# Optimization experiments

Hardware: AMD Instinct MI355X
Metric: run time of the kernel (lower is better)

The kernel has to match this reference:

```python
import jax, jax.numpy as jnp
import numpy as np

B, C, IC, H, W = 16, 256, 128, 32, 32  # batch, in_channels, inter_channels, spatial
EPS = 1e-5


def _conv1x1(x, w, b=None):
    # x: [B,C,H,W], w: [O,C] -> [B,O,H,W]
    y = jnp.einsum('bchw,oc->bohw', x, w)
    if b is not None:
        y = y + b[None, :, None, None]
    return y


def _dot_kernel(x, wt, wp):
    # relu-matmul attention, symmetrized, degree-rsqrt normalized with zero masking
    b, _, h, w = x.shape
    n = h * w
    t = jnp.maximum(_conv1x1(x, wt), 0.0).reshape(b, -1, n)  # [B,IC,N]
    p = jnp.maximum(_conv1x1(x, wp), 0.0).reshape(b, -1, n)  # [B,IC,N]
    att = jnp.einsum('bcn,bcm->bnm', t, p)                    # [B,N,N]
    att = (att + att.transpose(0, 2, 1)) * 0.5
    d = att.sum(axis=2)                                       # [B,N]
    dinv = jnp.where(d != 0, jax.lax.rsqrt(jnp.where(d != 0, d, 1.0)), 0.0)
    return att * dinv[:, None, :] * dinv[:, :, None]


def _bn(x, gamma, beta):
    # BatchNorm2d in training mode (batch statistics, biased variance)
    mu = jnp.mean(x, axis=(0, 2, 3), keepdims=True)
    var = jnp.mean((x - mu) ** 2, axis=(0, 2, 3), keepdims=True)
    xhat = (x - mu) * jax.lax.rsqrt(var + EPS)
    return xhat * gamma[None, :, None, None] + beta[None, :, None, None]


def setup_inputs() -> dict:
    key = jax.random.key(0)
    ks = jax.random.split(key, 32)
    s = 0.05
    inp = {
        'x':  jax.random.normal(ks[0], (B, C, H, W), jnp.float32),
        'ob': jax.random.normal(ks[1], (B, C, H, W), jnp.float32),
        'od': jax.random.normal(ks[2], (B, C, H, W), jnp.float32),
        'Wt': jax.random.normal(ks[3], (IC, C), jnp.float32) * s,
        'Wp': jax.random.normal(ks[4], (IC, C), jnp.float32) * s,
        'Wgx': jax.random.normal(ks[5], (IC, C), jnp.float32) * s,
        'bgx': jax.random.normal(ks[6], (IC,), jnp.float32) * s,
        'Wgb': jax.random.normal(ks[7], (IC, C), jnp.float32) * s,
        'bgb': jax.random.normal(ks[8], (IC,), jnp.float32) * s,
        'Wgd': jax.random.normal(ks[9], (IC, C), jnp.float32) * s,
        'bgd': jax.random.normal(ks[10], (IC,), jnp.float32) * s,
        'Wwx': jax.random.normal(ks[11], (C, IC), jnp.float32) * s,
        'bwx': jax.random.normal(ks[12], (C,), jnp.float32) * s,
        'Wwb': jax.random.normal(ks[13], (C, IC), jnp.float32) * s,
        'bwb': jax.random.normal(ks[14], (C,), jnp.float32) * s,
        'Wwd': jax.random.normal(ks[15], (C, IC), jnp.float32) * s,
        'bwd': jax.random.normal(ks[16], (C,), jnp.float32) * s,
        'Wwxb': jax.random.normal(ks[17], (C, IC), jnp.float32) * s,
        'bwxb': jax.random.normal(ks[18], (C,), jnp.float32) * s,
        'Wwxd': jax.random.normal(ks[19], (C, IC), jnp.float32) * s,
        'bwxd': jax.random.normal(ks[20], (C,), jnp.float32) * s,
        'gamma1': jnp.ones((C,), jnp.float32),
        'beta1': jnp.zeros((C,), jnp.float32),
        'gamma2': jnp.ones((C,), jnp.float32),
        'beta2': jnp.zeros((C,), jnp.float32),
        'Wout': jax.random.normal(ks[21], (C, C), jnp.float32) * s,
        'bout': jax.random.normal(ks[22], (C,), jnp.float32) * s,
    }
    return inp


def reference(x, ob, od, Wt, Wp, Wgx, bgx, Wgb, bgb, Wgd, bgd,
              Wwx, bwx, Wwb, bwb, Wwd, bwd, Wwxb, bwxb, Wwxd, bwxd,
              gamma1, beta1, gamma2, beta2, Wout, bout):
    b, c, h, w = x.shape
    n = h * w

    def g_tokens(inp, wg, bg):
        return _conv1x1(inp, wg, bg).reshape(b, -1, n).transpose(0, 2, 1)  # [B,N,IC]

    g_x = g_tokens(x, Wgx, bgx)
    g_b = g_tokens(ob, Wgb, bgb)
    g_d = g_tokens(od, Wgd, bgd)

    f_x = _dot_kernel(x, Wt, Wp)
    f_b = _dot_kernel(ob, Wt, Wp)
    f_d = _dot_kernel(od, Wt, Wp)

    def agg(f, g):
        # bmm(f,g).transpose(1,2).view(B,IC,H,W)
        return jnp.einsum('bnm,bmi->bin', f, g).reshape(b, -1, h, w)

    x_self = _conv1x1(agg(f_x, g_x), Wwx, bwx)
    ob_self = _conv1x1(agg(f_b, g_b), Wwb, bwb)
    od_self = _conv1x1(agg(f_d, g_d), Wwd, bwd)
    x_ob_cross = _conv1x1(agg(f_b, g_x), Wwxb, bwxb)
    x_od_cross = _conv1x1(agg(f_d, g_x), Wwxd, bwxd)

    od_final = _bn(od_self + x_ob_cross, gamma1, beta1)
    ob_final = _bn(ob_self + x_od_cross, gamma2, beta2)
    output = _conv1x1(od_final + ob_final + x_self, Wout, bout)
    return output + x
```

## Files before the change

kernel.cpp:

```cpp
#include <hip/hip_runtime.h>

#define GAS __attribute__((address_space(1)))
#define LAS __attribute__((address_space(3)))

typedef __attribute__((ext_vector_type(8))) short short8;
typedef __attribute__((ext_vector_type(4))) short short4_t;
typedef __attribute__((ext_vector_type(4))) float f32x4;
typedef unsigned short u16;

constexpr int cB = 16, cC = 256, cIC = 128, cN = 1024;

__device__ __forceinline__ u16 f2bf(float v) {
    unsigned u = __builtin_bit_cast(unsigned, v);
    return (u16)((u + 0x7fffu + ((u >> 16) & 1u)) >> 16);
}
__device__ __forceinline__ float bf2f(u16 v) {
    unsigned u = ((unsigned)v) << 16;
    return __builtin_bit_cast(float, u);
}
__device__ __forceinline__ float rsz(float d) {
    return (d != 0.0f) ? rsqrtf(d) : 0.0f;
}

template<int N> __device__ __forceinline__ void wait_vmcnt() {
    if constexpr (N == 0) asm volatile("s_waitcnt vmcnt(0)" ::: "memory");
    else if constexpr (N == 1) asm volatile("s_waitcnt vmcnt(1)" ::: "memory");
    else if constexpr (N == 2) asm volatile("s_waitcnt vmcnt(2)" ::: "memory");
    else if constexpr (N == 3) asm volatile("s_waitcnt vmcnt(3)" ::: "memory");
    else if constexpr (N == 4) asm volatile("s_waitcnt vmcnt(4)" ::: "memory");
    else if constexpr (N == 5) asm volatile("s_waitcnt vmcnt(5)" ::: "memory");
    else if constexpr (N == 6) asm volatile("s_waitcnt vmcnt(6)" ::: "memory");
    else if constexpr (N == 8) asm volatile("s_waitcnt vmcnt(8)" ::: "memory");
}

template<int BM, int BN, int WR, int WC, bool BREMAP = false>
__device__ __forceinline__ void gemm_core(
    const u16* __restrict__ Ab, const u16* __restrict__ Ab2, int ksplit, int lda,
    const u16* __restrict__ Bb, int ldb, int K,
    u16* lsA, u16* lsB,
    f32x4 (&acc)[BM/(WR*16)][BN/(WC*16)])
{
    constexpr int THREADS = WR * WC * 64;
    constexpr int MR = BM / (WR * 16), NR = BN / (WC * 16);
    constexpr int ACH = (BM * 64) / (THREADS * 16);
    constexpr int BCH = (BN * 64) / (THREADS * 16);
    constexpr int RPC = THREADS / 4;
    constexpr int ISSUES = ACH + BCH;

    const int tid  = threadIdx.x;
    const int lane = tid & 63;
    const int wave = tid >> 6;
    const int wr = wave / WC, wc = wave % WC;
    const int r0 = tid >> 2, slot = tid & 3;

    auto stage = [&](int buf, int kk) {
        const u16* Ak = (Ab2 != nullptr && kk >= ksplit) ? (Ab2 + (kk - ksplit)) : (Ab + kk);
        const u16* Bk = Bb + (BREMAP ? (((kk >> 7) << 8) + (kk & 127)) : kk);
        #pragma unroll
        for (int c = 0; c < ACH; c++) {
            int row = c * RPC + r0;
            int sk = (slot ^ ((row >> 1) & 3)) << 3;
            __builtin_amdgcn_global_load_lds((GAS void*)(Ak + (size_t)row * lda + sk),
                (LAS void*)(lsA + buf * (BM * 32) + c * (THREADS * 8) + (wave << 9)), 16, 0, 0);
        }
        #pragma unroll
        for (int c = 0; c < BCH; c++) {
            int row = c * RPC + r0;
            int sk = (slot ^ ((row >> 1) & 3)) << 3;
            __builtin_amdgcn_global_load_lds((GAS void*)(Bk + (size_t)row * ldb + sk),
                (LAS void*)(lsB + buf * (BN * 32) + c * (THREADS * 8) + (wave << 9)), 16, 0, 0);
        }
    };

    stage(0, 0);
    const int nt = K >> 5;
    for (int t = 0; t < nt; t++) {
        const int cur = t & 1;
        if (t + 1 < nt) { stage(cur ^ 1, (t + 1) << 5); wait_vmcnt<ISSUES>(); }
        else            wait_vmcnt<0>();
        __builtin_amdgcn_s_barrier();
        asm volatile("" ::: "memory");

        const u16* la = lsA + cur * (BM * 32);
        const u16* lb = lsB + cur * (BN * 32);
        short8 af[MR], bf[NR];
        #pragma unroll
        for (int m = 0; m < MR; m++) {
            int row = wr * (BM / WR) + (m << 4) + (lane & 15);
            af[m] = *(const short8*)&la[(row << 5) + (((lane >> 4) ^ ((row >> 1) & 3)) << 3)];
        }
        #pragma unroll
        for (int n = 0; n < NR; n++) {
            int row = wc * (BN / WC) + (n << 4) + (lane & 15);
            bf[n] = *(const short8*)&lb[(row << 5) + (((lane >> 4) ^ ((row >> 1) & 3)) << 3)];
        }
        #pragma unroll
        for (int m = 0; m < MR; m++)
            #pragma unroll
            for (int n = 0; n < NR; n++)
                acc[m][n] = __builtin_amdgcn_mfma_f32_16x16x32_bf16(af[m], bf[n], acc[m][n], 0, 0, 0);

        asm volatile("s_waitcnt lgkmcnt(0)" ::: "memory");
        __builtin_amdgcn_sched_barrier(0);
        __builtin_amdgcn_s_barrier();
    }
}

template<int BM, int BN, int WR, int WC, bool RELU, bool OBF16, bool RBIAS, bool RESID>
__global__ __launch_bounds__(WR*WC*64) void gemm_bt(
    const u16* __restrict__ A, long long sA, long long sA2, int lda,
    const u16* __restrict__ B, long long sB, long long sB2, int ldb,
    void* __restrict__ C, long long sC, long long sC2, int ldc,
    int K,
    const float* __restrict__ bias, int sb2,
    const float* __restrict__ resid, long long sR)
{
    __shared__ alignas(16) u16 lsA[2 * BM * 32];
    __shared__ alignas(16) u16 lsB[2 * BN * 32];

    const int lane = threadIdx.x & 63;
    const int wave = threadIdx.x >> 6;
    const int wr = wave / WC, wc = wave % WC;
    const int zlo = blockIdx.z & 15, zhi = blockIdx.z >> 4;

    const u16* Ab = A + zlo * sA + zhi * sA2 + (size_t)(blockIdx.x * BM) * lda;
    const u16* Bb = B + zlo * sB + zhi * sB2 + (size_t)(blockIdx.y * BN) * ldb;

    f32x4 acc[BM/(WR*16)][BN/(WC*16)] = {};
    gemm_core<BM, BN, WR, WC>(Ab, nullptr, K, lda, Bb, ldb, K, lsA, lsB, acc);

    const int rowb = blockIdx.x * BM + wr * (BM / WR) + ((lane >> 4) << 2);
    const int colb = blockIdx.y * BN + wc * (BN / WC) + (lane & 15);
    const long long cbase = zlo * sC + zhi * sC2;
    #pragma unroll
    for (int m = 0; m < BM/(WR*16); m++) {
        #pragma unroll
        for (int n = 0; n < BN/(WC*16); n++) {
            #pragma unroll
            for (int r = 0; r < 4; r++) {
                int row = rowb + m * 16 + r;
                int col = colb + n * 16;
                float v = acc[m][n][r];
                if (RBIAS) v += bias[zhi * sb2 + row];
                if (RESID) v += resid[zlo * sR + (size_t)row * ldc + col];
                if (RELU)  v = fmaxf(v, 0.0f);
                if (OBF16) ((u16*)C)[cbase + (size_t)row * ldc + col] = f2bf(v);
                else       ((float*)C)[cbase + (size_t)row * ldc + col] = v;
            }
        }
    }
}

__global__ __launch_bounds__(512) void tp_gemm(
    const u16* __restrict__ XT, const u16* __restrict__ WTP,
    u16* __restrict__ TP, float* __restrict__ CS)
{
    __shared__ alignas(16) u16 lsA[2 * 128 * 32];
    __shared__ alignas(16) u16 lsB[2 * 256 * 32];

    const int nx = blockIdx.x, z = blockIdx.z;
    const u16* Ab = XT + (size_t)z * 262144 + (size_t)(nx * 128) * 256;

    f32x4 acc[4][4] = {};
    gemm_core<128, 256, 2, 4>(Ab, nullptr, 256, 256, WTP, 256, 256, lsA, lsB, acc);

    const int lane = threadIdx.x & 63;
    const int wave = threadIdx.x >> 6;
    const int wr = wave >> 2, wc = wave & 3;
    const int rowb = nx * 128 + wr * 64 + ((lane >> 4) << 2);
    const int colb = wc * 64 + (lane & 15);
    u16* Cb = TP + (size_t)z * 262144;

    float cp[4] = {};
    #pragma unroll
    for (int m = 0; m < 4; m++)
        #pragma unroll
        for (int n = 0; n < 4; n++)
            #pragma unroll
            for (int r = 0; r < 4; r++) {
                float v = fmaxf(acc[m][n][r], 0.0f);
                Cb[(size_t)(rowb + m * 16 + r) * 256 + colb + n * 16] = f2bf(v);
                cp[n] += v;
            }
    #pragma unroll
    for (int n = 0; n < 4; n++) {
        float v = cp[n];
        v += __shfl_xor(v, 16, 64);
        v += __shfl_xor(v, 32, 64);
        if (lane < 16)
            atomicAdd(&CS[z * 256 + colb + n * 16], v);
    }
}

__global__ __launch_bounds__(256) void tp_transpose(
    const u16* __restrict__ TP, const float* __restrict__ CS,
    u16* __restrict__ TPt, float* __restrict__ DINV)
{
    __shared__ u16 ls[64][68];
    __shared__ float ws[64];
    __shared__ float pd[4][64];

    const int z = blockIdx.z;
    const int n0 = blockIdx.x << 6, c0 = blockIdx.y << 6;
    const int tid = threadIdx.x;

    if (tid < 64) ws[tid] = 0.5f * CS[z * 256 + ((c0 + tid) ^ 128)];

    const u16* src = TP + (size_t)z * 262144;
    #pragma unroll
    for (int p = 0; p < 2; p++) {
        int nl = p * 32 + (tid >> 3);
        int c8 = (tid & 7) << 3;
        short8 v = *(const short8*)&src[(size_t)(n0 + nl) * 256 + c0 + c8];
        #pragma unroll
        for (int j = 0; j < 8; j++) ls[c8 + j][nl] = (u16)v[j];
    }
    __syncthreads();

    u16* dst = TPt + (size_t)z * 262144;
    #pragma unroll
    for (int p = 0; p < 2; p++) {
        int cl = p * 32 + (tid >> 3);
        int n8 = (tid & 7) << 3;
        short4_t o0, o1;
        #pragma unroll
        for (int j = 0; j < 4; j++) { o0[j] = (short)ls[cl][n8 + j]; o1[j] = (short)ls[cl][n8 + 4 + j]; }
        *(short4_t*)&dst[(size_t)(c0 + cl) * 1024 + n0 + n8] = o0;
        *(short4_t*)&dst[(size_t)(c0 + cl) * 1024 + n0 + n8 + 4] = o1;
    }

    const int n = tid & 63, q = tid >> 6;
    float a = 0;
    #pragma unroll
    for (int c = 0; c < 16; c++) a += bf2f(ls[q * 16 + c][n]) * ws[q * 16 + c];
    pd[q][n] = a;
    __syncthreads();
    if (tid < 64)
        atomicAdd(&DINV[(z << 10) + n0 + tid],
                  pd[0][tid] + pd[1][tid] + pd[2][tid] + pd[3][tid]);
}

__global__ __launch_bounds__(256) void g_gemm(
    const u16* __restrict__ XT, const u16* __restrict__ WG,
    const float* __restrict__ BG, const float* __restrict__ DINV,
    u16* __restrict__ GXp, u16* __restrict__ GBp, u16* __restrict__ GDp)
{
    __shared__ alignas(16) u16 lsA[2 * 128 * 32];
    __shared__ alignas(16) u16 lsB[2 * 128 * 32];

    const int yb = blockIdx.x, zs = blockIdx.z;
    const int stream = zs >> 4, b = zs & 15;

    const u16* Ab = WG + stream * 32768;
    const u16* Bb = XT + (size_t)zs * 262144 + (size_t)(yb * 128) * 256;

    f32x4 acc[4][4] = {};
    gemm_core<128, 128, 2, 2>(Ab, nullptr, 256, 256, Bb, 256, 256, lsA, lsB, acc);

    const int lane = threadIdx.x & 63;
    const int wave = threadIdx.x >> 6;
    const int wr = wave >> 1, wc = wave & 1;
    const int rowb = (wr << 6) + ((lane >> 4) << 2);
    const int colb = yb * 128 + (wc << 6) + (lane & 15);
    const float* dvx = DINV + (b << 10);
    const float* dvb = DINV + 16384 + (b << 10);
    const float* dvd = DINV + 32768 + (b << 10);
    float sx[4], sb_[4], sd[4];
    #pragma unroll
    for (int n = 0; n < 4; n++) {
        int col = colb + n * 16;
        if (stream == 0) { sx[n] = rsz(dvx[col]); sb_[n] = rsz(dvb[col]); sd[n] = rsz(dvd[col]); }
        else if (stream == 1) sb_[n] = rsz(dvb[col]);
        else sd[n] = rsz(dvd[col]);
    }
    #pragma unroll
    for (int m = 0; m < 4; m++) {
        #pragma unroll
        for (int r = 0; r < 4; r++) {
            int row = rowb + m * 16 + r;
            float bias = BG[stream * 128 + row];
            #pragma unroll
            for (int n = 0; n < 4; n++) {
                int col = colb + n * 16;
                float v = acc[m][n][r] + bias;
                if (stream == 0) {
                    GXp[(size_t)b * 131072 + ((size_t)row << 10) + col] = f2bf(v * sx[n]);
                    GBp[(size_t)b * 262144 + ((size_t)(row + 128) << 10) + col] = f2bf(v * sb_[n]);
                    GDp[(size_t)b * 262144 + ((size_t)(row + 128) << 10) + col] = f2bf(v * sd[n]);
                } else if (stream == 1) {
                    GBp[(size_t)b * 262144 + ((size_t)row << 10) + col] = f2bf(v * sb_[n]);
                } else {
                    GDp[(size_t)b * 262144 + ((size_t)row << 10) + col] = f2bf(v * sd[n]);
                }
            }
        }
    }
}

__global__ __launch_bounds__(256) void inner_splitk(
    const u16* __restrict__ TPt, const u16* __restrict__ GXp,
    const u16* __restrict__ GBp, const u16* __restrict__ GDp,
    u16* __restrict__ MX, u16* __restrict__ MB, u16* __restrict__ MD)
{
    __shared__ alignas(16) u16 lsA[2 * 128 * 32];
    __shared__ alignas(16) u16 lsB[2 * 128 * 32];

    const int bz = blockIdx.z;
    const int split = bz / 48, z = bz % 48;
    const int which = z >> 4, b = z & 15;
    if (which == 0 && blockIdx.y) return;
    const u16* Gp = (which == 0) ? GXp : (which == 1) ? GBp : GDp;
    u16* M = (which == 0) ? MX : (which == 1) ? MB : MD;
    const int JD  = (which == 0) ? 128 : 256;
    const int ldc = 2 * JD;
    const long long sB = (which == 0) ? 131072 : 262144;

    const u16* Ab = TPt + (size_t)z * 262144 + (size_t)(blockIdx.x * 128) * 1024 + split * 512;
    const u16* Bb = Gp + (size_t)b * sB + (size_t)(blockIdx.y * 128) * 1024 + split * 512;

    f32x4 acc[4][4] = {};
    gemm_core<128, 128, 2, 2>(Ab, nullptr, 512, 1024, Bb, 1024, 512, lsA, lsB, acc);

    const int lane = threadIdx.x & 63;
    const int wave = threadIdx.x >> 6;
    const int wr = wave >> 1, wc = wave & 1;
    const int rowb = blockIdx.x * 128 + (wr << 6) + ((lane >> 4) << 2);
    const int colb = blockIdx.y * 128 + (wc << 6) + (lane & 15);
    u16* Cb = M + (size_t)b * (256 * ldc);
    #pragma unroll
    for (int m = 0; m < 4; m++)
        #pragma unroll
        for (int n = 0; n < 4; n++)
            #pragma unroll
            for (int r = 0; r < 4; r++) {
                int row = (rowb + m * 16 + r) ^ 128;
                int col = split * JD + colb + n * 16;
                Cb[(size_t)row * ldc + col] = f2bf(acc[m][n][r]);
            }
}

__global__ __launch_bounds__(512) void fold_gemm(
    const u16* __restrict__ WF2, const u16* __restrict__ MX,
    const u16* __restrict__ MB, const u16* __restrict__ MD,
    u16* __restrict__ FF2)
{
    __shared__ alignas(16) u16 lsA[2 * 128 * 32];
    __shared__ alignas(16) u16 lsB[2 * 256 * 32];

    const int z = blockIdx.z, q = z >> 4, b = z & 15;
    const int pr = (q == 4) ? 2 : (q >> 1);
    const int side = (q == 1 || q == 3) ? 1 : 0;

    const u16* Ab = WF2 + q * 65536 + (size_t)(blockIdx.x * 128) * 256;

    f32x4 acc[4][4] = {};
    if (q == 4) {
        const u16* Bb = MX + (size_t)b * 65536;
        gemm_core<128, 256, 2, 4, false>(Ab, nullptr, 256, 256, Bb, 256, 256, lsA, lsB, acc);
    } else {
        const u16* Mp = (q == 1 || q == 2) ? MB : MD;
        const int coff = side ? 128 : 0;
        const u16* Bb = Mp + (size_t)b * 131072 + coff;
        gemm_core<128, 256, 2, 4, true>(Ab, nullptr, 256, 256, Bb, 512, 256, lsA, lsB, acc);
    }

    const int lane = threadIdx.x & 63;
    const int wave = threadIdx.x >> 6;
    const int wr = wave >> 2, wc = wave & 3;
    const int rowb = blockIdx.x * 128 + wr * 64 + ((lane >> 4) << 2);
    const int colb = wc * 64 + (lane & 15);
    u16* Cb = FF2 + (size_t)pr * 2097152 + (size_t)b * 131072;
    #pragma unroll
    for (int m = 0; m < 4; m++)
        #pragma unroll
        for (int n = 0; n < 4; n++)
            #pragma unroll
            for (int r = 0; r < 4; r++)
                Cb[(size_t)(rowb + m * 16 + r) * 512 + side * 256 + colb + n * 16]
                    = f2bf(acc[m][n][r]);
}

__global__ __launch_bounds__(512) void outer_gemm(
    const u16* __restrict__ TP, const u16* __restrict__ FF2,
    const float* __restrict__ DINV,
    u16* __restrict__ SALL, float* __restrict__ BNA)
{
    __shared__ alignas(16) u16 lsA[2 * 128 * 32];
    __shared__ alignas(16) u16 lsB[2 * 256 * 32];

    const int z = blockIdx.z, zhi = z >> 4, b = z & 15;
    const int sa1[3] = {2, 1, 0}, sa2[3] = {1, 2, 0};

    const int lane = threadIdx.x & 63;
    const int wave = threadIdx.x >> 6;
    const int wr = wave >> 2, wc = wave & 3;
    const int rowb = blockIdx.x * 128 + wr * 64 + ((lane >> 4) << 2);
    const int colb = wc * 64 + (lane & 15);

    const u16* A1 = TP + (size_t)(sa1[zhi] * 16 + b) * 262144 + (size_t)(blockIdx.x * 128) * 256;
    const u16* B1 = FF2 + (size_t)zhi * 2097152 + (size_t)b * 131072;
    const float* dv1 = DINV + sa1[zhi] * 16384 + (b << 10);

    f32x4 acc[4][4] = {};
    gemm_core<128, 256, 2, 4>(A1, nullptr, 256, 256, B1, 512, 256, lsA, lsB, acc);

    f32x4 keep[4][4];
    #pragma unroll
    for (int m = 0; m < 4; m++) {
        f32x4 dva;
        #pragma unroll
        for (int r = 0; r < 4; r++) dva[r] = rsz(dv1[rowb + m * 16 + r]);
        #pragma unroll
        for (int n = 0; n < 4; n++) keep[m][n] = acc[m][n] * dva;
    }

    if (zhi < 2) {
        const u16* A2 = TP + (size_t)(sa2[zhi] * 16 + b) * 262144 + (size_t)(blockIdx.x * 128) * 256;
        const u16* B2 = B1 + 256;
        const float* dv2 = DINV + sa2[zhi] * 16384 + (b << 10);
        #pragma unroll
        for (int m = 0; m < 4; m++)
            #pragma unroll
            for (int n = 0; n < 4; n++) acc[m][n] = f32x4{0.f, 0.f, 0.f, 0.f};
        gemm_core<128, 256, 2, 4>(A2, nullptr, 256, 256, B2, 512, 256, lsA, lsB, acc);
        #pragma unroll
        for (int m = 0; m < 4; m++) {
            f32x4 dva;
            #pragma unroll
            for (int r = 0; r < 4; r++) dva[r] = rsz(dv2[rowb + m * 16 + r]);
            #pragma unroll
            for (int n = 0; n < 4; n++) keep[m][n] = keep[m][n] + acc[m][n] * dva;
        }
    }

    u16* Cb = SALL + (size_t)b * 786432;
    float csum[4] = {}, csq[4] = {};
    #pragma unroll
    for (int m = 0; m < 4; m++)
        #pragma unroll
        for (int n = 0; n < 4; n++)
            #pragma unroll
            for (int r = 0; r < 4; r++) {
                float v = keep[m][n][r];
                Cb[(size_t)(rowb + m * 16 + r) * 768 + zhi * 256 + colb + n * 16] = f2bf(v);
                csum[n] += v;
                csq[n] += v * v;
            }
    if (zhi < 2) {
        #pragma unroll
        for (int n = 0; n < 4; n++) {
            float s = csum[n], q = csq[n];
            s += __shfl_xor(s, 16, 64); s += __shfl_xor(s, 32, 64);
            q += __shfl_xor(q, 16, 64); q += __shfl_xor(q, 32, 64);
            if (lane < 16) {
                atomicAdd(&BNA[zhi * 512 + colb + n * 16], s);
                atomicAdd(&BNA[zhi * 512 + 256 + colb + n * 16], q);
            }
        }
    }
}

__global__ __launch_bounds__(256) void bnscale(
    const float* __restrict__ Wout, const float* __restrict__ g1, const float* __restrict__ be1,
    const float* __restrict__ g2, const float* __restrict__ be2,
    const float* __restrict__ bwx, const float* __restrict__ bout,
    const float* __restrict__ BNA, u16* __restrict__ WoutS, float* __restrict__ BIAS2)
{
    int o = blockIdx.x, c = threadIdx.x;
    const float inv = 1.0f / 16384.0f;
    float m1 = BNA[c] * inv;
    float v1 = BNA[256 + c] * inv - m1 * m1;
    float sc1 = g1[c] * rsqrtf(v1 + 1e-5f), sh1 = be1[c] - m1 * sc1;
    float m2 = BNA[512 + c] * inv;
    float v2 = BNA[768 + c] * inv - m2 * m2;
    float sc2 = g2[c] * rsqrtf(v2 + 1e-5f), sh2 = be2[c] - m2 * sc2;
    float wv = Wout[o * 256 + c];
    WoutS[o * 768 + c]       = f2bf(wv * sc1);
    WoutS[o * 768 + 256 + c] = f2bf(wv * sc2);
    WoutS[o * 768 + 512 + c] = f2bf(wv);
    __shared__ float red[256];
    red[c] = wv * (sh1 + sh2 + bwx[c]);
    __syncthreads();
    for (int s = 128; s; s >>= 1) { if (c < s) red[c] += red[c + s]; __syncthreads(); }
    if (c == 0) BIAS2[o] = red[0] + bout[o];
}

__global__ __launch_bounds__(256) void prep_transpose(
    const float* __restrict__ x, const float* __restrict__ ob,
    const float* __restrict__ od, u16* __restrict__ xt,
    const float* Wt, const float* Wp,
    const float* Wgx, const float* Wgb, const float* Wgd,
    const float* bgx, const float* bgb, const float* bgd,
    const float* Wwd, const float* Wwxb, const float* Wwb,
    const float* Wwxd, const float* Wwx,
    u16* wtp, u16* wg, u16* wf2, float* bg,
    float* __restrict__ ZZ)
{
    const int tid = threadIdx.x;
    if (blockIdx.z == 48) {
        int base = (blockIdx.y * 16 + blockIdx.x) * 1024;
        #pragma unroll
        for (int l = 0; l < 4; l++) {
            int t = base + l * 256 + tid;
            wtp[t] = f2bf(t < 32768 ? Wt[t] : Wp[t - 32768]);
            if (t < 32768) {
                wg[t] = f2bf(Wgx[t]); wg[32768 + t] = f2bf(Wgb[t]); wg[65536 + t] = f2bf(Wgd[t]);
            }
            {
                int o = t >> 8, k = t & 255, j = k & 127;
                const float* Wq[5] = {Wwd, Wwxb, Wwb, Wwxd, Wwx};
                #pragma unroll
                for (int q = 0; q < 5; q++)
                    wf2[q * 65536 + t] = f2bf(0.5f * Wq[q][o * 128 + j]);
            }
            if (t < 384) bg[t] = (t < 128) ? bgx[t] : (t < 256) ? bgb[t - 128] : bgd[t - 256];
            if (t < 62464) ZZ[t] = 0.0f;
        }
        return;
    }
    __shared__ float ls[64][68];
    const int z = blockIdx.z, which = z >> 4, b = z & 15;
    const float* src = (which == 0) ? x : (which == 1) ? ob : od;
    const float* s = src + (size_t)b * cC * cN;
    u16* dst = xt + (size_t)z * (cN * cC);
    const int n0 = blockIdx.x << 6, c0 = blockIdx.y << 6;

    const int cl0 = tid >> 4, n4 = (tid & 15) << 2;
    #pragma unroll
    for (int p = 0; p < 4; p++) {
        int cl = cl0 + (p << 4);
        f32x4 v = *(const f32x4*)&s[(size_t)(c0 + cl) * cN + n0 + n4];
        ls[cl][n4] = v[0]; ls[cl][n4 + 1] = v[1]; ls[cl][n4 + 2] = v[2]; ls[cl][n4 + 3] = v[3];
    }
    __syncthreads();
    const int nl0 = tid >> 3, c8 = (tid & 7) << 3;
    #pragma unroll
    for (int q = 0; q < 2; q++) {
        int nl = nl0 + (q << 5);
        short8 o;
        #pragma unroll
        for (int j = 0; j < 8; j++) o[j] = (short)f2bf(ls[c8 + j][nl]);
        *(short8*)&dst[(size_t)(n0 + nl) * 256 + c0 + c8] = o;
    }
}

extern "C" void kernel_launch(void* const* d_in, const int* in_sizes, int n_in,
                              void* d_out, int out_size, void* d_ws, size_t ws_size,
                              hipStream_t stream)
{
    const float* x    = (const float*)d_in[0];
    const float* ob   = (const float*)d_in[1];
    const float* od   = (const float*)d_in[2];
    const float* Wt   = (const float*)d_in[3];
    const float* Wp   = (const float*)d_in[4];
    const float* Wgx  = (const float*)d_in[5];
    const float* bgx  = (const float*)d_in[6];
    const float* Wgb  = (const float*)d_in[7];
    const float* bgb  = (const float*)d_in[8];
    const float* Wgd  = (const float*)d_in[9];
    const float* bgd  = (const float*)d_in[10];
    const float* Wwx  = (const float*)d_in[11];
    const float* bwx  = (const float*)d_in[12];
    const float* Wwb  = (const float*)d_in[13];
    const float* Wwd  = (const float*)d_in[15];
    const float* Wwxb = (const float*)d_in[17];
    const float* Wwxd = (const float*)d_in[19];
    const float* g1   = (const float*)d_in[21];
    const float* be1  = (const float*)d_in[22];
    const float* g2   = (const float*)d_in[23];
    const float* be2  = (const float*)d_in[24];
    const float* Wout = (const float*)d_in[25];
    const float* bout = (const float*)d_in[26];
    float* out = (float*)d_out;

    char* w = (char*)d_ws;
    u16*   XT    = (u16*)(w);
    u16*   TPt   = (u16*)(w + 25165824);
    u16*   TP    = (u16*)(w + 50331648);
    u16*   GXp   = (u16*)(w + 75497472);
    u16*   GBp   = (u16*)(w + 79691776);
    u16*   GDp   = (u16*)(w + 88080384);
    u16*   MX    = (u16*)(w + 96468992);
    u16*   MB    = (u16*)(w + 98566144);
    u16*   MD    = (u16*)(w + 102760448);
    u16*   FF2   = (u16*)(w + 106954752);
    u16*   WTP   = (u16*)(w + 119537664);
    u16*   WG    = (u16*)(w + 119668736);
    u16*   WF2   = (u16*)(w + 119865344);
    u16*   WoutS = (u16*)(w + 120520704);
    float* BGf   = (float*)(w + 120913920);
    float* BIAS2 = (float*)(w + 120915968);
    float* ZZ    = (float*)(w + 120920064);

    float* CS   = ZZ;
    float* BNA  = ZZ + 12288;
    float* DINV = ZZ + 13312;
    u16*   SALL = TPt;

    prep_transpose<<<dim3(16, 4, 49), 256, 0, stream>>>(
        x, ob, od, XT, Wt, Wp, Wgx, Wgb, Wgd, bgx, bgb, bgd,
        Wwd, Wwxb, Wwb, Wwxd, Wwx, WTP, WG, WF2, BGf, ZZ);

    tp_gemm<<<dim3(8, 1, 48), 512, 0, stream>>>(XT, WTP, TP, CS);

    tp_transpose<<<dim3(16, 4, 48), 256, 0, stream>>>(TP, CS, TPt, DINV);

    g_gemm<<<dim3(8, 1, 48), 256, 0, stream>>>(XT, WG, BGf, DINV, GXp, GBp, GDp);

    inner_splitk<<<dim3(2, 2, 96), 256, 0, stream>>>(TPt, GXp, GBp, GDp, MX, MB, MD);

    fold_gemm<<<dim3(2, 1, 80), 512, 0, stream>>>(WF2, MX, MB, MD, FF2);

    outer_gemm<<<dim3(8, 1, 48), 512, 0, stream>>>(TP, FF2, DINV, SALL, BNA);

    bnscale<<<dim3(256), 256, 0, stream>>>(Wout, g1, be1, g2, be2, bwx, bout,
                                           BNA, WoutS, BIAS2);

    gemm_bt<128, 128, 2, 2, false, false, true, true><<<dim3(2, 8, 16), 256, 0, stream>>>(
        WoutS, 0, 0, 768,  SALL, 786432, 0, 768,  out, 262144, 0, 1024,
        768, BIAS2, 0, x, 262144);
}
```

Before: 145.3 us.

## Fold degree normalization into transposed T/P buffers and split-K final GEMM with atomics

The per-row degree scale is now applied once, in a new per-row-tile transpose kernel that computes the full channel dot product locally. That kernel writes pre-scaled T/P in both layouts, which removes the DINV atomics, the scaling epilogues in g_gemm and outer_gemm, and lets outer_gemm run one fused two-source GEMM. The final output GEMM is split along K into two halves that atomically add into an output buffer pre-seeded with x during the prep pass, which doubles the block count. The trade-offs are extra bf16 rounding of the scaled operands, an extra full copy of x to the output, and atomic-add traffic on the output.

```diff
diff --git a/kernel.cpp b/kernel.cpp
--- a/kernel.cpp
+++ b/kernel.cpp
@@ -4,7 +4,6 @@
 #define LAS __attribute__((address_space(3)))
 
 typedef __attribute__((ext_vector_type(8))) short short8;
-typedef __attribute__((ext_vector_type(4))) short short4_t;
 typedef __attribute__((ext_vector_type(4))) float f32x4;
 typedef unsigned short u16;
 
@@ -106,51 +105,6 @@
     }
 }
 
-template<int BM, int BN, int WR, int WC, bool RELU, bool OBF16, bool RBIAS, bool RESID>
-__global__ __launch_bounds__(WR*WC*64) void gemm_bt(
-    const u16* __restrict__ A, long long sA, long long sA2, int lda,
-    const u16* __restrict__ B, long long sB, long long sB2, int ldb,
-    void* __restrict__ C, long long sC, long long sC2, int ldc,
-    int K,
-    const float* __restrict__ bias, int sb2,
-    const float* __restrict__ resid, long long sR)
-{
-    __shared__ alignas(16) u16 lsA[2 * BM * 32];
-    __shared__ alignas(16) u16 lsB[2 * BN * 32];
-
-    const int lane = threadIdx.x & 63;
-    const int wave = threadIdx.x >> 6;
-    const int wr = wave / WC, wc = wave % WC;
-    const int zlo = blockIdx.z & 15, zhi = blockIdx.z >> 4;
-
-    const u16* Ab = A + zlo * sA + zhi * sA2 + (size_t)(blockIdx.x * BM) * lda;
-    const u16* Bb = B + zlo * sB + zhi * sB2 + (size_t)(blockIdx.y * BN) * ldb;
-
-    f32x4 acc[BM/(WR*16)][BN/(WC*16)] = {};
-    gemm_core<BM, BN, WR, WC>(Ab, nullptr, K, lda, Bb, ldb, K, lsA, lsB, acc);
-
-    const int rowb = blockIdx.x * BM + wr * (BM / WR) + ((lane >> 4) << 2);
-    const int colb = blockIdx.y * BN + wc * (BN / WC) + (lane & 15);
-    const long long cbase = zlo * sC + zhi * sC2;
-    #pragma unroll
-    for (int m = 0; m < BM/(WR*16); m++) {
-        #pragma unroll
-        for (int n = 0; n < BN/(WC*16); n++) {
-            #pragma unroll
-            for (int r = 0; r < 4; r++) {
-                int row = rowb + m * 16 + r;
-                int col = colb + n * 16;
-                float v = acc[m][n][r];
-                if (RBIAS) v += bias[zhi * sb2 + row];
-                if (RESID) v += resid[zlo * sR + (size_t)row * ldc + col];
-                if (RELU)  v = fmaxf(v, 0.0f);
-                if (OBF16) ((u16*)C)[cbase + (size_t)row * ldc + col] = f2bf(v);
-                else       ((float*)C)[cbase + (size_t)row * ldc + col] = v;
-            }
-        }
-    }
-}
-
 __global__ __launch_bounds__(512) void tp_gemm(
     const u16* __restrict__ XT, const u16* __restrict__ WTP,
     u16* __restrict__ TP, float* __restrict__ CS)
@@ -192,64 +146,82 @@
     }
 }
 
-__global__ __launch_bounds__(256) void tp_transpose(
+__global__ __launch_bounds__(256) void tpt2(
     const u16* __restrict__ TP, const float* __restrict__ CS,
-    u16* __restrict__ TPt, float* __restrict__ DINV)
-{
-    __shared__ u16 ls[64][68];
-    __shared__ float ws[64];
-    __shared__ float pd[4][64];
+    u16* __restrict__ TPS, u16* __restrict__ TPSt)
+{
+    __shared__ u16 ls[64][264];
+    __shared__ float ws[256];
+    __shared__ float pd[64][4];
+    __shared__ float dvs[64];
 
     const int z = blockIdx.z;
-    const int n0 = blockIdx.x << 6, c0 = blockIdx.y << 6;
+    const int n0 = blockIdx.x << 6;
     const int tid = threadIdx.x;
 
-    if (tid < 64) ws[tid] = 0.5f * CS[z * 256 + ((c0 + tid) ^ 128)];
+    ws[tid] = 0.5f * CS[z * 256 + (tid ^ 128)];
 
     const u16* src = TP + (size_t)z * 262144;
     #pragma unroll
-    for (int p = 0; p < 2; p++) {
-        int nl = p * 32 + (tid >> 3);
-        int c8 = (tid & 7) << 3;
-        short8 v = *(const short8*)&src[(size_t)(n0 + nl) * 256 + c0 + c8];
-        #pragma unroll
-        for (int j = 0; j < 8; j++) ls[c8 + j][nl] = (u16)v[j];
+    for (int k = 0; k < 8; k++) {
+        int chunk = k * 256 + tid;
+        int row = chunk >> 5, c8 = (chunk & 31) << 3;
+        *(short8*)&ls[row][c8] = *(const short8*)&src[(size_t)(n0 + row) * 256 + c8];
     }
     __syncthreads();
 
-    u16* dst = TPt + (size_t)z * 262144;
-    #pragma unroll
-    for (int p = 0; p < 2; p++) {
-        int cl = p * 32 + (tid >> 3);
-        int n8 = (tid & 7) << 3;
-        short4_t o0, o1;
-        #pragma unroll
-        for (int j = 0; j < 4; j++) { o0[j] = (short)ls[cl][n8 + j]; o1[j] = (short)ls[cl][n8 + 4 + j]; }
-        *(short4_t*)&dst[(size_t)(c0 + cl) * 1024 + n0 + n8] = o0;
-        *(short4_t*)&dst[(size_t)(c0 + cl) * 1024 + n0 + n8 + 4] = o1;
-    }
-
-    const int n = tid & 63, q = tid >> 6;
-    float a = 0;
-    #pragma unroll
-    for (int c = 0; c < 16; c++) a += bf2f(ls[q * 16 + c][n]) * ws[q * 16 + c];
-    pd[q][n] = a;
+    {
+        const int row = tid >> 2, q = tid & 3;
+        float a = 0;
+        #pragma unroll 16
+        for (int i = 0; i < 64; i++) {
+            int c = q * 64 + i;
+            a += bf2f(ls[row][c]) * ws[c];
+        }
+        pd[row][q] = a;
+    }
     __syncthreads();
-    if (tid < 64)
-        atomicAdd(&DINV[(z << 10) + n0 + tid],
-                  pd[0][tid] + pd[1][tid] + pd[2][tid] + pd[3][tid]);
+    if (tid < 64) {
+        float d = pd[tid][0] + pd[tid][1] + pd[tid][2] + pd[tid][3];
+        dvs[tid] = rsz(d);
+    }
+    __syncthreads();
+
+    u16* So = TPS + (size_t)z * 262144;
+    #pragma unroll
+    for (int k = 0; k < 8; k++) {
+        int chunk = k * 256 + tid;
+        int row = chunk >> 5, c8 = (chunk & 31) << 3;
+        short8 v = *(const short8*)&ls[row][c8];
+        float s = dvs[row];
+        short8 o;
+        #pragma unroll
+        for (int j = 0; j < 8; j++) o[j] = (short)f2bf(bf2f((u16)v[j]) * s);
+        *(short8*)&So[(size_t)(n0 + row) * 256 + c8] = o;
+    }
+
+    u16* To = TPSt + (size_t)z * 262144 + (size_t)tid * 1024 + n0;
+    #pragma unroll
+    for (int jb = 0; jb < 8; jb++) {
+        short8 o;
+        #pragma unroll
+        for (int j = 0; j < 8; j++) {
+            int n = jb * 8 + j;
+            o[j] = (short)f2bf(bf2f(ls[n][tid]) * dvs[n]);
+        }
+        *(short8*)&To[jb * 8] = o;
+    }
 }
 
 __global__ __launch_bounds__(256) void g_gemm(
     const u16* __restrict__ XT, const u16* __restrict__ WG,
-    const float* __restrict__ BG, const float* __restrict__ DINV,
-    u16* __restrict__ GXp, u16* __restrict__ GBp, u16* __restrict__ GDp)
+    const float* __restrict__ BG, u16* __restrict__ G)
 {
     __shared__ alignas(16) u16 lsA[2 * 128 * 32];
     __shared__ alignas(16) u16 lsB[2 * 128 * 32];
 
     const int yb = blockIdx.x, zs = blockIdx.z;
-    const int stream = zs >> 4, b = zs & 15;
+    const int stream = zs >> 4;
 
     const u16* Ab = WG + stream * 32768;
     const u16* Bb = XT + (size_t)zs * 262144 + (size_t)(yb * 128) * 256;
@@ -262,44 +234,21 @@
     const int wr = wave >> 1, wc = wave & 1;
     const int rowb = (wr << 6) + ((lane >> 4) << 2);
     const int colb = yb * 128 + (wc << 6) + (lane & 15);
-    const float* dvx = DINV + (b << 10);
-    const float* dvb = DINV + 16384 + (b << 10);
-    const float* dvd = DINV + 32768 + (b << 10);
-    float sx[4], sb_[4], sd[4];
-    #pragma unroll
-    for (int n = 0; n < 4; n++) {
-        int col = colb + n * 16;
-        if (stream == 0) { sx[n] = rsz(dvx[col]); sb_[n] = rsz(dvb[col]); sd[n] = rsz(dvd[col]); }
-        else if (stream == 1) sb_[n] = rsz(dvb[col]);
-        else sd[n] = rsz(dvd[col]);
-    }
-    #pragma unroll
-    for (int m = 0; m < 4; m++) {
+    u16* Gz = G + ((size_t)zs << 17);
+    #pragma unroll
+    for (int m = 0; m < 4; m++)
         #pragma unroll
         for (int r = 0; r < 4; r++) {
             int row = rowb + m * 16 + r;
             float bias = BG[stream * 128 + row];
             #pragma unroll
-            for (int n = 0; n < 4; n++) {
-                int col = colb + n * 16;
-                float v = acc[m][n][r] + bias;
-                if (stream == 0) {
-                    GXp[(size_t)b * 131072 + ((size_t)row << 10) + col] = f2bf(v * sx[n]);
-                    GBp[(size_t)b * 262144 + ((size_t)(row + 128) << 10) + col] = f2bf(v * sb_[n]);
-                    GDp[(size_t)b * 262144 + ((size_t)(row + 128) << 10) + col] = f2bf(v * sd[n]);
-                } else if (stream == 1) {
-                    GBp[(size_t)b * 262144 + ((size_t)row << 10) + col] = f2bf(v * sb_[n]);
-                } else {
-                    GDp[(size_t)b * 262144 + ((size_t)row << 10) + col] = f2bf(v * sd[n]);
-                }
-            }
-        }
-    }
+            for (int n = 0; n < 4; n++)
+                Gz[((size_t)row << 10) + colb + n * 16] = f2bf(acc[m][n][r] + bias);
+        }
 }
 
 __global__ __launch_bounds__(256) void inner_splitk(
-    const u16* __restrict__ TPt, const u16* __restrict__ GXp,
-    const u16* __restrict__ GBp, const u16* __restrict__ GDp,
+    const u16* __restrict__ TPSt, const u16* __restrict__ G,
     u16* __restrict__ MX, u16* __restrict__ MB, u16* __restrict__ MD)
 {
     __shared__ alignas(16) u16 lsA[2 * 128 * 32];
@@ -309,14 +258,13 @@
     const int split = bz / 48, z = bz % 48;
     const int which = z >> 4, b = z & 15;
     if (which == 0 && blockIdx.y) return;
-    const u16* Gp = (which == 0) ? GXp : (which == 1) ? GBp : GDp;
     u16* M = (which == 0) ? MX : (which == 1) ? MB : MD;
     const int JD  = (which == 0) ? 128 : 256;
     const int ldc = 2 * JD;
-    const long long sB = (which == 0) ? 131072 : 262144;
-
-    const u16* Ab = TPt + (size_t)z * 262144 + (size_t)(blockIdx.x * 128) * 1024 + split * 512;
-    const u16* Bb = Gp + (size_t)b * sB + (size_t)(blockIdx.y * 128) * 1024 + split * 512;
+    const int srcz = blockIdx.y ? b : (which * 16 + b);
+
+    const u16* Ab = TPSt + (size_t)z * 262144 + (size_t)(blockIdx.x * 128) * 1024 + split * 512;
+    const u16* Bb = G + ((size_t)srcz << 17) + split * 512;
 
     f32x4 acc[4][4] = {};
     gemm_core<128, 128, 2, 2>(Ab, nullptr, 512, 1024, Bb, 1024, 512, lsA, lsB, acc);
@@ -381,8 +329,7 @@
 }
 
 __global__ __launch_bounds__(512) void outer_gemm(
-    const u16* __restrict__ TP, const u16* __restrict__ FF2,
-    const float* __restrict__ DINV,
+    const u16* __restrict__ TPS, const u16* __restrict__ FF2,
     u16* __restrict__ SALL, float* __restrict__ BNA)
 {
     __shared__ alignas(16) u16 lsA[2 * 128 * 32];
@@ -390,6 +337,15 @@
 
     const int z = blockIdx.z, zhi = z >> 4, b = z & 15;
     const int sa1[3] = {2, 1, 0}, sa2[3] = {1, 2, 0};
+    const int K = (zhi == 2) ? 256 : 512;
+
+    const u16* A1 = TPS + (size_t)(sa1[zhi] * 16 + b) * 262144 + (size_t)(blockIdx.x * 128) * 256;
+    const u16* A2 = (zhi == 2) ? nullptr
+                  : TPS + (size_t)(sa2[zhi] * 16 + b) * 262144 + (size_t)(blockIdx.x * 128) * 256;
+    const u16* Bb = FF2 + (size_t)zhi * 2097152 + (size_t)b * 131072;
+
+    f32x4 acc[4][4] = {};
+    gemm_core<128, 256, 2, 4>(A1, A2, 256, 256, Bb, 512, K, lsA, lsB, acc);
 
     const int lane = threadIdx.x & 63;
     const int wave = threadIdx.x >> 6;
@@ -397,42 +353,6 @@
     const int rowb = blockIdx.x * 128 + wr * 64 + ((lane >> 4) << 2);
     const int colb = wc * 64 + (lane & 15);
 
-    const u16* A1 = TP + (size_t)(sa1[zhi] * 16 + b) * 262144 + (size_t)(blockIdx.x * 128) * 256;
-    const u16* B1 = FF2 + (size_t)zhi * 2097152 + (size_t)b * 131072;
-    const float* dv1 = DINV + sa1[zhi] * 16384 + (b << 10);
-
-    f32x4 acc[4][4] = {};
-    gemm_core<128, 256, 2, 4>(A1, nullptr, 256, 256, B1, 512, 256, lsA, lsB, acc);
-
-    f32x4 keep[4][4];
-    #pragma unroll
-    for (int m = 0; m < 4; m++) {
-        f32x4 dva;
-        #pragma unroll
-        for (int r = 0; r < 4; r++) dva[r] = rsz(dv1[rowb + m * 16 + r]);
-        #pragma unroll
-        for (int n = 0; n < 4; n++) keep[m][n] = acc[m][n] * dva;
-    }
-
-    if (zhi < 2) {
-        const u16* A2 = TP + (size_t)(sa2[zhi] * 16 + b) * 262144 + (size_t)(blockIdx.x * 128) * 256;
-        const u16* B2 = B1 + 256;
-        const float* dv2 = DINV + sa2[zhi] * 16384 + (b << 10);
-        #pragma unroll
-        for (int m = 0; m < 4; m++)
-            #pragma unroll
-            for (int n = 0; n < 4; n++) acc[m][n] = f32x4{0.f, 0.f, 0.f, 0.f};
-        gemm_core<128, 256, 2, 4>(A2, nullptr, 256, 256, B2, 512, 256, lsA, lsB, acc);
-        #pragma unroll
-        for (int m = 0; m < 4; m++) {
-            f32x4 dva;
-            #pragma unroll
-            for (int r = 0; r < 4; r++) dva[r] = rsz(dv2[rowb + m * 16 + r]);
-            #pragma unroll
-            for (int n = 0; n < 4; n++) keep[m][n] = keep[m][n] + acc[m][n] * dva;
-        }
-    }
-
     u16* Cb = SALL + (size_t)b * 786432;
     float csum[4] = {}, csq[4] = {};
     #pragma unroll
@@ -441,7 +361,7 @@
         for (int n = 0; n < 4; n++)
             #pragma unroll
             for (int r = 0; r < 4; r++) {
-                float v = keep[m][n][r];
+                float v = acc[m][n][r];
                 Cb[(size_t)(rowb + m * 16 + r) * 768 + zhi * 256 + colb + n * 16] = f2bf(v);
                 csum[n] += v;
                 csq[n] += v * v;
@@ -485,6 +405,41 @@
     if (c == 0) BIAS2[o] = red[0] + bout[o];
 }
 
+__global__ __launch_bounds__(256) void final_split(
+    const u16* __restrict__ WoutS, const u16* __restrict__ SALL,
+    const float* __restrict__ BIAS2, float* __restrict__ out)
+{
+    __shared__ alignas(16) u16 lsA[2 * 128 * 32];
+    __shared__ alignas(16) u16 lsB[2 * 128 * 32];
+
+    const int split = blockIdx.z >> 4, b = blockIdx.z & 15;
+    const int xb = blockIdx.x, yb = blockIdx.y;
+
+    const u16* Ab = WoutS + (size_t)(xb * 128) * 768 + split * 384;
+    const u16* Bb = SALL + (size_t)b * 786432 + (size_t)(yb * 128) * 768 + split * 384;
+
+    f32x4 acc[4][4] = {};
+    gemm_core<128, 128, 2, 2>(Ab, nullptr, 384, 768, Bb, 768, 384, lsA, lsB, acc);
+
+    const int lane = threadIdx.x & 63;
+    const int wave = threadIdx.x >> 6;
+    const int wr = wave >> 1, wc = wave & 1;
+    const int rowb = xb * 128 + (wr << 6) + ((lane >> 4) << 2);
+    const int colb = yb * 128 + (wc << 6) + (lane & 15);
+    #pragma unroll
+    for (int m = 0; m < 4; m++)
+        #pragma unroll
+        for (int n = 0; n < 4; n++)
+            #pragma unroll
+            for (int r = 0; r < 4; r++) {
+                int row = rowb + m * 16 + r;
+                int col = colb + n * 16;
+                float v = acc[m][n][r];
+                if (split == 0) v += BIAS2[row];
+                atomicAdd(&out[(size_t)b * 262144 + (size_t)row * 1024 + col], v);
+            }
+}
+
 __global__ __launch_bounds__(256) void prep_transpose(
     const float* __restrict__ x, const float* __restrict__ ob,
     const float* __restrict__ od, u16* __restrict__ xt,
@@ -494,7 +449,7 @@
     const float* Wwd, const float* Wwxb, const float* Wwb,
     const float* Wwxd, const float* Wwx,
     u16* wtp, u16* wg, u16* wf2, float* bg,
-    float* __restrict__ ZZ)
+    float* __restrict__ ZZ, float* __restrict__ outp)
 {
     const int tid = threadIdx.x;
     if (blockIdx.z == 48) {
@@ -514,7 +469,7 @@
                     wf2[q * 65536 + t] = f2bf(0.5f * Wq[q][o * 128 + j]);
             }
             if (t < 384) bg[t] = (t < 128) ? bgx[t] : (t < 256) ? bgb[t - 128] : bgd[t - 256];
-            if (t < 62464) ZZ[t] = 0.0f;
+            if (t < 13312) ZZ[t] = 0.0f;
         }
         return;
     }
@@ -523,6 +478,7 @@
     const float* src = (which == 0) ? x : (which == 1) ? ob : od;
     const float* s = src + (size_t)b * cC * cN;
     u16* dst = xt + (size_t)z * (cN * cC);
+    float* ox = outp + (size_t)b * (cC * cN);
     const int n0 = blockIdx.x << 6, c0 = blockIdx.y << 6;
 
     const int cl0 = tid >> 4, n4 = (tid & 15) << 2;
@@ -530,6 +486,7 @@
     for (int p = 0; p < 4; p++) {
         int cl = cl0 + (p << 4);
         f32x4 v = *(const f32x4*)&s[(size_t)(c0 + cl) * cN + n0 + n4];
+        if (which == 0) *(f32x4*)&ox[(size_t)(c0 + cl) * cN + n0 + n4] = v;
         ls[cl][n4] = v[0]; ls[cl][n4 + 1] = v[1]; ls[cl][n4 + 2] = v[2]; ls[cl][n4 + 3] = v[3];
     }
     __syncthreads();
@@ -575,48 +532,44 @@
 
     char* w = (char*)d_ws;
     u16*   XT    = (u16*)(w);
-    u16*   TPt   = (u16*)(w + 25165824);
-    u16*   TP    = (u16*)(w + 50331648);
-    u16*   GXp   = (u16*)(w + 75497472);
-    u16*   GBp   = (u16*)(w + 79691776);
-    u16*   GDp   = (u16*)(w + 88080384);
-    u16*   MX    = (u16*)(w + 96468992);
-    u16*   MB    = (u16*)(w + 98566144);
-    u16*   MD    = (u16*)(w + 102760448);
-    u16*   FF2   = (u16*)(w + 106954752);
-    u16*   WTP   = (u16*)(w + 119537664);
-    u16*   WG    = (u16*)(w + 119668736);
-    u16*   WF2   = (u16*)(w + 119865344);
-    u16*   WoutS = (u16*)(w + 120520704);
-    float* BGf   = (float*)(w + 120913920);
-    float* BIAS2 = (float*)(w + 120915968);
-    float* ZZ    = (float*)(w + 120920064);
+    u16*   TP    = (u16*)(w + 25165824);
+    u16*   TPS   = (u16*)(w + 50331648);
+    u16*   TPSt  = (u16*)(w + 75497472);
+    u16*   G     = (u16*)(w + 100663296);
+    u16*   MX    = (u16*)(w + 113246208);
+    u16*   MB    = (u16*)(w + 115343360);
+    u16*   MD    = (u16*)(w + 119537664);
+    u16*   FF2   = (u16*)(w + 123731968);
+    u16*   WTP   = (u16*)(w + 136314880);
+    u16*   WG    = (u16*)(w + 136445952);
+    u16*   WF2   = (u16*)(w + 136642560);
+    u16*   WoutS = (u16*)(w + 137297920);
+    float* BGf   = (float*)(w + 137691136);
+    float* BIAS2 = (float*)(w + 137693184);
+    float* ZZ    = (float*)(w + 137697280);
 
     float* CS   = ZZ;
     float* BNA  = ZZ + 12288;
-    float* DINV = ZZ + 13312;
-    u16*   SALL = TPt;
+    u16*   SALL = TP;
 
     prep_transpose<<<dim3(16, 4, 49), 256, 0, stream>>>(
         x, ob, od, XT, Wt, Wp, Wgx, Wgb, Wgd, bgx, bgb, bgd,
-        Wwd, Wwxb, Wwb, Wwxd, Wwx, WTP, WG, WF2, BGf, ZZ);
+        Wwd, Wwxb, Wwb, Wwxd, Wwx, WTP, WG, WF2, BGf, ZZ, out);
 
     tp_gemm<<<dim3(8, 1, 48), 512, 0, stream>>>(XT, WTP, TP, CS);
 
-    tp_transpose<<<dim3(16, 4, 48), 256, 0, stream>>>(TP, CS, TPt, DINV);
-
-    g_gemm<<<dim3(8, 1, 48), 256, 0, stream>>>(XT, WG, BGf, DINV, GXp, GBp, GDp);
-
-    inner_splitk<<<dim3(2, 2, 96), 256, 0, stream>>>(TPt, GXp, GBp, GDp, MX, MB, MD);
+    tpt2<<<dim3(16, 1, 48), 256, 0, stream>>>(TP, CS, TPS, TPSt);
+
+    g_gemm<<<dim3(8, 1, 48), 256, 0, stream>>>(XT, WG, BGf, G);
+
+    inner_splitk<<<dim3(2, 2, 96), 256, 0, stream>>>(TPSt, G, MX, MB, MD);
 
     fold_gemm<<<dim3(2, 1, 80), 512, 0, stream>>>(WF2, MX, MB, MD, FF2);
 
-    outer_gemm<<<dim3(8, 1, 48), 512, 0, stream>>>(TP, FF2, DINV, SALL, BNA);
+    outer_gemm<<<dim3(8, 1, 48), 512, 0, stream>>>(TPS, FF2, SALL, BNA);
 
     bnscale<<<dim3(256), 256, 0, stream>>>(Wout, g1, be1, g2, be2, bwx, bout,
                                            BNA, WoutS, BIAS2);
 
-    gemm_bt<128, 128, 2, 2, false, false, true, true><<<dim3(2, 8, 16), 256, 0, stream>>>(
-        WoutS, 0, 0, 768,  SALL, 786432, 0, 768,  out, 262144, 0, 1024,
-        768, BIAS2, 0, x, 262144);
-}
+    final_split<<<dim3(2, 8, 32), 256, 0, stream>>>(WoutS, SALL, BIAS2, out);
+}
```

Measured after the change: 169.3 us. 16.5% more time.
